# Kernel optimization log

Hardware: AMD Instinct MI355X
Metric: run time of the kernel (lower is better)

## Reference

```python
import jax, jax.numpy as jnp
import numpy as np

B, N, E, H = 32, 1024, 1024, 8
D = E // H      # head_dim = 128, att_mid_dim = [128, 64, 128]
MID = 64


def setup_inputs() -> dict:
    key = jax.random.key(0)
    ks = jax.random.split(key, 12)

    def lin(k, out_d, in_d):
        return (jax.random.normal(k, (out_d, in_d), jnp.float32) * 0.02,
                jnp.zeros((out_d,), jnp.float32))

    Wq, bq = lin(ks[0], E, E)
    Wk, bk = lin(ks[1], E, E)
    Wv, bv = lin(ks[2], E, E)
    Wb, bb = lin(ks[3], MID, D)    # attention_basic: Linear(mid[0]=D -> mid[1]=64) + ReLU
    Wl, bl = lin(ks[4], 1, MID)    # attention_last: Linear(64 -> 1)
    Wl2, bl2 = lin(ks[5], D, MID)  # attention_last2: Linear(64 -> D)
    query = jax.random.normal(ks[6], (B, E), jnp.float32)
    k_in = jax.random.normal(ks[7], (B, N, E), jnp.float32)
    value1 = jax.random.normal(ks[8], (B, E), jnp.float32)
    value2 = jax.random.normal(ks[9], (B, N, E), jnp.float32)
    mask = jax.random.randint(ks[10], (B, N), 0, 2, jnp.int32)
    mask = mask.at[:, 0].set(1)  # guarantee at least one valid position per row
    return {"query": query, "key": k_in, "mask": mask, "value1": value1,
            "value2": value2, "Wq": Wq, "bq": bq, "Wk": Wk, "bk": bk,
            "Wv": Wv, "bv": bv, "Wb": Wb, "bb": bb, "Wl": Wl, "bl": bl,
            "Wl2": Wl2, "bl2": bl2}


def reference(query, key, mask, value1, value2, Wq, bq, Wk, bk, Wv, bv,
              Wb, bb, Wl, bl, Wl2, bl2):
    # --- QKV projections (single-query attention) ---
    Q = (query @ Wq.T + bq).reshape(B, 1, H, D).transpose(0, 2, 1, 3)    # [B,H,1,D]
    K = (key @ Wk.T + bk).reshape(B, N, H, D).transpose(0, 2, 1, 3)      # [B,H,N,D]
    V = (key @ Wv.T + bv).reshape(B, N, H, D).transpose(0, 2, 1, 3)      # [B,H,N,D]
    v1 = value1.reshape(B, H, D)                                          # [B,H,D]
    v2 = (value2 @ Wv.T + bv).reshape(B, N, H, D).transpose(0, 2, 1, 3)   # [B,H,N,D]

    scores = jnp.einsum('bhqd,bhkd->bhqk', Q, K) / jnp.sqrt(jnp.float32(D))  # [B,H,1,N]
    attended = jnp.einsum('bhqk,bhkd->bhqd', scores, V)                      # [B,H,1,D]
    attn_map = jnp.broadcast_to(attended, (B, H, N, D))                      # expand(-1,-1,N,-1)

    # --- SCAtt attn_net ---
    h = jax.nn.relu(jnp.einsum('bhnd,md->bhnm', attn_map, Wb) + bb)          # [B,H,N,64]
    mf = mask.astype(h.dtype)                                                # [B,N]
    mext = mf[:, None, :, None]                                              # [B,1,N,1]
    att_map_pool = jnp.sum(h * mext, axis=2) / jnp.sum(mext, axis=2)         # [B,H,64]
    alpha_spatial = (jnp.einsum('bhnm,om->bhno', h, Wl) + bl)[..., 0]        # [B,H,N]
    alpha_channel = jax.nn.sigmoid(att_map_pool @ Wl2.T + bl2)               # [B,H,D]
    alpha_spatial = jnp.where(mf[:, None, :] == 0, jnp.float32(-1e9), alpha_spatial)
    alpha_spatial = jax.nn.softmax(alpha_spatial, axis=-1)                   # [B,H,N]
    v2_att = jnp.einsum('bhn,bhnd->bhd', alpha_spatial, v2)                  # [B,H,D]
    attn = v1 * v2_att * alpha_channel                                       # [B,H,D]
    return attn.reshape(B, H * D)
```

## Files before the change

kernel.cpp:

```cpp
#include <hip/hip_runtime.h>

#define B_  32
#define N_  1024
#define E_  1024
#define H_  8
#define D_  128
#define MID_ 64
#define NT_  16
#define TR_  64
#define NS2_ 16


__global__ __launch_bounds__(256) void k_qkproj(
        const float* __restrict__ query, const float* __restrict__ Wq,
        const float* __restrict__ bq, const float* __restrict__ Wk,
        const float* __restrict__ bk, float* __restrict__ qk,
        float* __restrict__ qb)
{
    const int bh = blockIdx.x;
    const int b = bh >> 3, h = bh & 7;
    const int t = threadIdx.x;

    __shared__ float Qp[2][D_];
    __shared__ float Qs[D_];
    __shared__ float red[2];

    {
        const int d = t & 127, half = t >> 7;
        const int row = h * D_ + d;
        const float4* wr = (const float4*)(Wq + (size_t)row * E_) + half * 128;
        const float4* qr = (const float4*)(query + (size_t)b * E_) + half * 128;
        float acc = 0.f;
        for (int i = 0; i < 128; ++i) {
            float4 w = wr[i], q = qr[i];
            acc += w.x * q.x + w.y * q.y + w.z * q.z + w.w * q.w;
        }
        Qp[half][d] = acc;
    }
    __syncthreads();
    if (t < D_) {
        const int row = h * D_ + t;
        float q = Qp[0][t] + Qp[1][t] + bq[row];
        Qs[t] = q;
        float qp = q * bk[row];
        #pragma unroll
        for (int off = 32; off; off >>= 1) qp += __shfl_down(qp, off);
        if ((t & 63) == 0) red[t >> 6] = qp;
    }
    __syncthreads();
    if (t == 0) qb[bh] = red[0] + red[1];

    const int e0 = t * 4;
    float4 a = make_float4(0.f, 0.f, 0.f, 0.f);
    const float* wkb = Wk + (size_t)(h * D_) * E_ + e0;
    for (int d = 0; d < D_; ++d) {
        float Qd = Qs[d];
        float4 w = *(const float4*)(wkb + (size_t)d * E_);
        a.x += Qd * w.x; a.y += Qd * w.y; a.z += Qd * w.z; a.w += Qd * w.w;
    }
    *(float4*)(qk + (size_t)bh * E_ + e0) = a;
}

__global__ __launch_bounds__(256) void k_scorepool(
        const float* __restrict__ key, const float* __restrict__ qk,
        const float* __restrict__ qb, float* __restrict__ PP,
        float* __restrict__ ssum)
{
    const int tile = blockIdx.x, b = blockIdx.y;
    const int t = threadIdx.x;
    const int c = t & 31, g = t >> 5;

    __shared__ __align__(16) float qks[H_ * E_];
    __shared__ __align__(16) float ssc[TR_][H_];

    {
        const float4* src = (const float4*)(qk + (size_t)b * H_ * E_);
        float4* dst = (float4*)qks;
        #pragma unroll
        for (int k = 0; k < 8; ++k) dst[t + k * 256] = src[t + k * 256];
    }
    __syncthreads();

    const float scale = 0.08838834764831845f;
    const float* keyb = key + ((size_t)b * N_ + (size_t)tile * TR_) * E_;
    const float4* qks4 = (const float4*)qks;
    const float qbv = qb[b * 8 + (c & 7)];

    float tsum = 0.f;
    #pragma unroll
    for (int p = 0; p < 2; ++p) {
        float acc[H_][4];
        #pragma unroll
        for (int h = 0; h < H_; ++h)
            #pragma unroll
            for (int j = 0; j < 4; ++j) acc[h][j] = 0.f;

        const float4* kr[4];
        #pragma unroll
        for (int j = 0; j < 4; ++j)
            kr[j] = (const float4*)(keyb + (size_t)(p * 32 + g * 4 + j) * E_);

        #pragma unroll 4
        for (int i = 0; i < 8; ++i) {
            float4 kf[4];
            #pragma unroll
            for (int j = 0; j < 4; ++j) kf[j] = kr[j][i * 32 + c];
            #pragma unroll
            for (int h = 0; h < H_; ++h) {
                float4 qf = qks4[h * 256 + i * 32 + c];
                #pragma unroll
                for (int j = 0; j < 4; ++j) {
                    acc[h][j] += qf.x * kf[j].x + qf.y * kf[j].y
                               + qf.z * kf[j].z + qf.w * kf[j].w;
                }
            }
        }
        #pragma unroll
        for (int off = 16; off; off >>= 1) {
            #pragma unroll
            for (int h = 0; h < H_; ++h)
                #pragma unroll
                for (int j = 0; j < 4; ++j)
                    acc[h][j] += __shfl_xor(acc[h][j], off);
        }
        const int r0 = p * 32 + g * 4;
        #pragma unroll
        for (int h = 0; h < H_; ++h) {
            if (c == h) {
                #pragma unroll
                for (int j = 0; j < 4; ++j) {
                    float s = (acc[h][j] + qbv) * scale;
                    ssc[r0 + j][h] = s;
                    tsum += s;
                }
            }
        }
    }
    if (c < H_) atomicAdd(&ssum[b * 8 + c], tsum);
    __syncthreads();

    {
        const int e0 = t * 4;
        float pacc[H_][4] = {};
        const float* kb = keyb + e0;
        #pragma unroll 4
        for (int n = 0; n < TR_; ++n) {
            float4 kv = *(const float4*)(kb + (size_t)n * E_);
            float4 s0 = *(const float4*)&ssc[n][0];
            float4 s1 = *(const float4*)&ssc[n][4];
            pacc[0][0] += s0.x * kv.x; pacc[0][1] += s0.x * kv.y;
            pacc[0][2] += s0.x * kv.z; pacc[0][3] += s0.x * kv.w;
            pacc[1][0] += s0.y * kv.x; pacc[1][1] += s0.y * kv.y;
            pacc[1][2] += s0.y * kv.z; pacc[1][3] += s0.y * kv.w;
            pacc[2][0] += s0.z * kv.x; pacc[2][1] += s0.z * kv.y;
            pacc[2][2] += s0.z * kv.z; pacc[2][3] += s0.z * kv.w;
            pacc[3][0] += s0.w * kv.x; pacc[3][1] += s0.w * kv.y;
            pacc[3][2] += s0.w * kv.z; pacc[3][3] += s0.w * kv.w;
            pacc[4][0] += s1.x * kv.x; pacc[4][1] += s1.x * kv.y;
            pacc[4][2] += s1.x * kv.z; pacc[4][3] += s1.x * kv.w;
            pacc[5][0] += s1.y * kv.x; pacc[5][1] += s1.y * kv.y;
            pacc[5][2] += s1.y * kv.z; pacc[5][3] += s1.y * kv.w;
            pacc[6][0] += s1.z * kv.x; pacc[6][1] += s1.z * kv.y;
            pacc[6][2] += s1.z * kv.z; pacc[6][3] += s1.z * kv.w;
            pacc[7][0] += s1.w * kv.x; pacc[7][1] += s1.w * kv.y;
            pacc[7][2] += s1.w * kv.z; pacc[7][3] += s1.w * kv.w;
        }
        #pragma unroll
        for (int h = 0; h < H_; ++h) {
            float* dst = PP + ((size_t)(b * H_) + h) * E_ + e0;
            atomicAdd(dst + 0, pacc[h][0]); atomicAdd(dst + 1, pacc[h][1]);
            atomicAdd(dst + 2, pacc[h][2]); atomicAdd(dst + 3, pacc[h][3]);
        }
    }
}

__global__ __launch_bounds__(256) void k_pool_v2(
        const float* __restrict__ value2, const int* __restrict__ mask,
        float* __restrict__ P2)
{
    const int ns = blockIdx.x, b = blockIdx.y;
    const int t = threadIdx.x, e0 = t * 4;
    const int n0 = ns * (N_ / NS2_);

    __shared__ int rows[N_ / NS2_];
    __shared__ int nrows;
    if (t == 0) nrows = 0;
    __syncthreads();
    if (t < N_ / NS2_) {
        if (mask[b * N_ + n0 + t]) {
            int idx = atomicAdd(&nrows, 1);
            rows[idx] = t;
        }
    }
    __syncthreads();
    const int nr = nrows;

    float a0 = 0.f, a1 = 0.f, a2 = 0.f, a3 = 0.f;
    const float* vb = value2 + ((size_t)(b * N_ + n0)) * E_ + e0;
    for (int i = 0; i < nr; ++i) {
        float4 v = *(const float4*)(vb + (size_t)rows[i] * E_);
        a0 += v.x; a1 += v.y; a2 += v.z; a3 += v.w;
    }
    float* dst = P2 + (size_t)b * E_ + e0;
    atomicAdd(dst + 0, a0); atomicAdd(dst + 1, a1);
    atomicAdd(dst + 2, a2); atomicAdd(dst + 3, a3);
}

__global__ __launch_bounds__(256) void k_final(
        const float* __restrict__ PP, const float* __restrict__ P2,
        const float* __restrict__ ssumg, const int* __restrict__ mask,
        const float* __restrict__ Wv, const float* __restrict__ bv,
        const float* __restrict__ Wb, const float* __restrict__ bb,
        const float* __restrict__ Wl2, const float* __restrict__ bl2,
        const float* __restrict__ value1, float* __restrict__ out)
{
    const int bh = blockIdx.x, b = bh >> 3, h = bh & 7;
    const int t = threadIdx.x;
    const int d = t & 127, half = t >> 7;

    __shared__ __align__(16) float pooled[E_];
    __shared__ __align__(16) float pool2[E_];
    __shared__ float attA[2][D_];
    __shared__ float attV[2][D_];
    __shared__ float att[D_];
    __shared__ float hv[MID_];
    __shared__ float red2[4];
    __shared__ float cnt_s;

    {
        const float4* pp = (const float4*)(PP + ((size_t)(b * H_) + h) * E_);
        const float4* p2 = (const float4*)(P2 + (size_t)b * E_);
        ((float4*)pooled)[t] = pp[t];
        ((float4*)pool2)[t]  = p2[t];

        int ci = 0;
        #pragma unroll
        for (int i = 0; i < 4; ++i) ci += mask[b * N_ + t + i * 256];
        float cf = (float)ci;
        #pragma unroll
        for (int off = 32; off; off >>= 1) cf += __shfl_down(cf, off);
        if ((t & 63) == 0) red2[t >> 6] = cf;
    }
    __syncthreads();
    if (t == 0) cnt_s = red2[0] + red2[1] + red2[2] + red2[3];

    const float ss = ssumg[bh];
    const float4* wv = (const float4*)(Wv + ((size_t)(h * D_ + d)) * E_) + half * 128;
    float accA = 0.f, accV = 0.f;
    #pragma unroll 4
    for (int i = 0; i < 128; ++i) {
        float4 w = wv[i];
        float4 pa = ((const float4*)pooled)[half * 128 + i];
        float4 pb = ((const float4*)pool2)[half * 128 + i];
        accA += pa.x * w.x + pa.y * w.y + pa.z * w.z + pa.w * w.w;
        accV += pb.x * w.x + pb.y * w.y + pb.z * w.z + pb.w * w.w;
    }
    attA[half][d] = accA;
    attV[half][d] = accV;
    __syncthreads();
    const float cnt = cnt_s;
    if (t < D_) att[t] = attA[0][t] + attA[1][t] + ss * bv[h * D_ + t];
    __syncthreads();
    if (t < MID_) {
        float a = bb[t];
        #pragma unroll 4
        for (int d2 = 0; d2 < D_; ++d2) a += att[d2] * Wb[t * D_ + d2];
        hv[t] = fmaxf(a, 0.f);
    }
    __syncthreads();
    if (t < D_) {
        float z = bl2[t];
        #pragma unroll
        for (int m = 0; m < MID_; ++m) z += hv[m] * Wl2[t * MID_ + m];
        float alphac = 1.f / (1.f + expf(-z));
        const float bvd = bv[h * D_ + t];
        float v2a = (attV[0][t] + attV[1][t]) / cnt + bvd;
        out[(size_t)b * E_ + h * D_ + t] =
            value1[(size_t)b * E_ + h * D_ + t] * v2a * alphac;
    }
}

extern "C" void kernel_launch(void* const* d_in, const int* in_sizes, int n_in,
                              void* d_out, int out_size, void* d_ws, size_t ws_size,
                              hipStream_t stream)
{
    const float* query  = (const float*)d_in[0];
    const float* key    = (const float*)d_in[1];
    const int*   mask   = (const int*)d_in[2];
    const float* value1 = (const float*)d_in[3];
    const float* value2 = (const float*)d_in[4];
    const float* Wq  = (const float*)d_in[5];
    const float* bq  = (const float*)d_in[6];
    const float* Wk  = (const float*)d_in[7];
    const float* bk  = (const float*)d_in[8];
    const float* Wv  = (const float*)d_in[9];
    const float* bv  = (const float*)d_in[10];
    const float* Wb  = (const float*)d_in[11];
    const float* bb  = (const float*)d_in[12];
    const float* Wl2 = (const float*)d_in[15];
    const float* bl2 = (const float*)d_in[16];
    float* out = (float*)d_out;

    char* ws = (char*)d_ws;
    const size_t OFF_P2 = (size_t)B_ * H_ * E_ * 4;
    const size_t OFF_SS = OFF_P2 + (size_t)B_ * E_ * 4;
    const size_t OFF_QB = OFF_SS + 1024;
    const size_t OFF_QK = OFF_QB + 1024;
    float* PP   = (float*)(ws);
    float* P2   = (float*)(ws + OFF_P2);
    float* ssum = (float*)(ws + OFF_SS);
    float* qb   = (float*)(ws + OFF_QB);
    float* qk   = (float*)(ws + OFF_QK);

    hipMemsetAsync(d_ws, 0, OFF_QB, stream);

    hipLaunchKernelGGL(k_qkproj, dim3(B_ * H_), dim3(256), 0, stream,
                       query, Wq, bq, Wk, bk, qk, qb);
    hipLaunchKernelGGL(k_scorepool, dim3(NT_, B_), dim3(256), 0, stream,
                       key, qk, qb, PP, ssum);
    hipLaunchKernelGGL(k_pool_v2, dim3(NS2_, B_), dim3(256), 0, stream,
                       value2, mask, P2);
    hipLaunchKernelGGL(k_final, dim3(B_ * H_), dim3(256), 0, stream,
                       PP, P2, ssum, mask, Wv, bv, Wb, bb, Wl2, bl2, value1, out);
}
```

Before: 437.5 us.

## Fuse v2 pooling into projection kernel, widen score tiles, coalesce final GEMV

Merges the value2 masked-pooling kernel into the Q/K projection kernel as extra blocks, so the two independent stages share one launch and can overlap. The score stage now computes 8 key rows per thread group in one pass instead of two passes of 4, which raises register pressure but reuses each shared-memory qk load across more rows. The final kernel's Wv GEMV is reorganised so 16 lanes read consecutive float4s of a row and reduce with shuffles, giving coalesced weight reads. Together these aim to cut launch overhead and memory stalls.

```diff
diff --git a/kernel.cpp b/kernel.cpp
--- a/kernel.cpp
+++ b/kernel.cpp
@@ -11,54 +11,90 @@
 #define NS2_ 16
 
 
-__global__ __launch_bounds__(256) void k_qkproj(
+__global__ __launch_bounds__(256) void k_pre(
         const float* __restrict__ query, const float* __restrict__ Wq,
         const float* __restrict__ bq, const float* __restrict__ Wk,
         const float* __restrict__ bk, float* __restrict__ qk,
-        float* __restrict__ qb)
+        float* __restrict__ qb,
+        const float* __restrict__ value2, const int* __restrict__ mask,
+        float* __restrict__ P2)
 {
-    const int bh = blockIdx.x;
-    const int b = bh >> 3, h = bh & 7;
     const int t = threadIdx.x;
 
     __shared__ float Qp[2][D_];
     __shared__ float Qs[D_];
     __shared__ float red[2];
-
-    {
-        const int d = t & 127, half = t >> 7;
-        const int row = h * D_ + d;
-        const float4* wr = (const float4*)(Wq + (size_t)row * E_) + half * 128;
-        const float4* qr = (const float4*)(query + (size_t)b * E_) + half * 128;
-        float acc = 0.f;
-        for (int i = 0; i < 128; ++i) {
-            float4 w = wr[i], q = qr[i];
-            acc += w.x * q.x + w.y * q.y + w.z * q.z + w.w * q.w;
-        }
-        Qp[half][d] = acc;
-    }
-    __syncthreads();
-    if (t < D_) {
-        const int row = h * D_ + t;
-        float q = Qp[0][t] + Qp[1][t] + bq[row];
-        Qs[t] = q;
-        float qp = q * bk[row];
-        #pragma unroll
-        for (int off = 32; off; off >>= 1) qp += __shfl_down(qp, off);
-        if ((t & 63) == 0) red[t >> 6] = qp;
-    }
-    __syncthreads();
-    if (t == 0) qb[bh] = red[0] + red[1];
-
-    const int e0 = t * 4;
-    float4 a = make_float4(0.f, 0.f, 0.f, 0.f);
-    const float* wkb = Wk + (size_t)(h * D_) * E_ + e0;
-    for (int d = 0; d < D_; ++d) {
-        float Qd = Qs[d];
-        float4 w = *(const float4*)(wkb + (size_t)d * E_);
-        a.x += Qd * w.x; a.y += Qd * w.y; a.z += Qd * w.z; a.w += Qd * w.w;
-    }
-    *(float4*)(qk + (size_t)bh * E_ + e0) = a;
+    __shared__ int rows[N_ / NS2_];
+    __shared__ int nrows;
+
+    if (blockIdx.x < 256) {
+        const int bh = blockIdx.x;
+        const int b = bh >> 3, h = bh & 7;
+
+        {
+            const int d = t & 127, half = t >> 7;
+            const int row = h * D_ + d;
+            const float4* wr = (const float4*)(Wq + (size_t)row * E_) + half * 128;
+            const float4* qr = (const float4*)(query + (size_t)b * E_) + half * 128;
+            float acc = 0.f;
+            #pragma unroll 8
+            for (int i = 0; i < 128; ++i) {
+                float4 w = wr[i], q = qr[i];
+                acc += w.x * q.x + w.y * q.y + w.z * q.z + w.w * q.w;
+            }
+            Qp[half][d] = acc;
+        }
+        __syncthreads();
+        if (t < D_) {
+            const int row = h * D_ + t;
+            float q = Qp[0][t] + Qp[1][t] + bq[row];
+            Qs[t] = q;
+            float qp = q * bk[row];
+            #pragma unroll
+            for (int off = 32; off; off >>= 1) qp += __shfl_down(qp, off);
+            if ((t & 63) == 0) red[t >> 6] = qp;
+        }
+        __syncthreads();
+        if (t == 0) qb[bh] = red[0] + red[1];
+
+        const int e0 = t * 4;
+        float4 a = make_float4(0.f, 0.f, 0.f, 0.f);
+        const float* wkb = Wk + (size_t)(h * D_) * E_ + e0;
+        #pragma unroll 8
+        for (int d = 0; d < D_; ++d) {
+            float Qd = Qs[d];
+            float4 w = *(const float4*)(wkb + (size_t)d * E_);
+            a.x += Qd * w.x; a.y += Qd * w.y; a.z += Qd * w.z; a.w += Qd * w.w;
+        }
+        *(float4*)(qk + (size_t)bh * E_ + e0) = a;
+    } else {
+        const int idx = blockIdx.x - 256;
+        const int b = idx & 31, ns = idx >> 5;
+        const int e0 = t * 4;
+        const int n0 = ns * (N_ / NS2_);
+
+        if (t == 0) nrows = 0;
+        __syncthreads();
+        if (t < N_ / NS2_) {
+            if (mask[b * N_ + n0 + t]) {
+                int i2 = atomicAdd(&nrows, 1);
+                rows[i2] = t;
+            }
+        }
+        __syncthreads();
+        const int nr = nrows;
+
+        float a0 = 0.f, a1 = 0.f, a2 = 0.f, a3 = 0.f;
+        const float* vb = value2 + ((size_t)(b * N_ + n0)) * E_ + e0;
+        #pragma unroll 4
+        for (int i = 0; i < nr; ++i) {
+            float4 v = *(const float4*)(vb + (size_t)rows[i] * E_);
+            a0 += v.x; a1 += v.y; a2 += v.z; a3 += v.w;
+        }
+        float* dst = P2 + (size_t)b * E_ + e0;
+        atomicAdd(dst + 0, a0); atomicAdd(dst + 1, a1);
+        atomicAdd(dst + 2, a2); atomicAdd(dst + 3, a3);
+    }
 }
 
 __global__ __launch_bounds__(256) void k_scorepool(
@@ -86,53 +122,49 @@
     const float4* qks4 = (const float4*)qks;
     const float qbv = qb[b * 8 + (c & 7)];
 
+    float acc[H_][8];
+    #pragma unroll
+    for (int h = 0; h < H_; ++h)
+        #pragma unroll
+        for (int j = 0; j < 8; ++j) acc[h][j] = 0.f;
+
+    const float4* kr[8];
+    #pragma unroll
+    for (int j = 0; j < 8; ++j)
+        kr[j] = (const float4*)(keyb + (size_t)(g * 8 + j) * E_);
+
+    #pragma unroll 2
+    for (int i = 0; i < 8; ++i) {
+        float4 kf[8];
+        #pragma unroll
+        for (int j = 0; j < 8; ++j) kf[j] = kr[j][i * 32 + c];
+        #pragma unroll
+        for (int h = 0; h < H_; ++h) {
+            float4 qf = qks4[h * 256 + i * 32 + c];
+            #pragma unroll
+            for (int j = 0; j < 8; ++j) {
+                acc[h][j] += qf.x * kf[j].x + qf.y * kf[j].y
+                           + qf.z * kf[j].z + qf.w * kf[j].w;
+            }
+        }
+    }
+    #pragma unroll
+    for (int off = 16; off; off >>= 1) {
+        #pragma unroll
+        for (int h = 0; h < H_; ++h)
+            #pragma unroll
+            for (int j = 0; j < 8; ++j)
+                acc[h][j] += __shfl_xor(acc[h][j], off);
+    }
     float tsum = 0.f;
     #pragma unroll
-    for (int p = 0; p < 2; ++p) {
-        float acc[H_][4];
-        #pragma unroll
-        for (int h = 0; h < H_; ++h)
+    for (int h = 0; h < H_; ++h) {
+        if (c == h) {
             #pragma unroll
-            for (int j = 0; j < 4; ++j) acc[h][j] = 0.f;
-
-        const float4* kr[4];
-        #pragma unroll
-        for (int j = 0; j < 4; ++j)
-            kr[j] = (const float4*)(keyb + (size_t)(p * 32 + g * 4 + j) * E_);
-
-        #pragma unroll 4
-        for (int i = 0; i < 8; ++i) {
-            float4 kf[4];
-            #pragma unroll
-            for (int j = 0; j < 4; ++j) kf[j] = kr[j][i * 32 + c];
-            #pragma unroll
-            for (int h = 0; h < H_; ++h) {
-                float4 qf = qks4[h * 256 + i * 32 + c];
-                #pragma unroll
-                for (int j = 0; j < 4; ++j) {
-                    acc[h][j] += qf.x * kf[j].x + qf.y * kf[j].y
-                               + qf.z * kf[j].z + qf.w * kf[j].w;
-                }
-            }
-        }
-        #pragma unroll
-        for (int off = 16; off; off >>= 1) {
-            #pragma unroll
-            for (int h = 0; h < H_; ++h)
-                #pragma unroll
-                for (int j = 0; j < 4; ++j)
-                    acc[h][j] += __shfl_xor(acc[h][j], off);
-        }
-        const int r0 = p * 32 + g * 4;
-        #pragma unroll
-        for (int h = 0; h < H_; ++h) {
-            if (c == h) {
-                #pragma unroll
-                for (int j = 0; j < 4; ++j) {
-                    float s = (acc[h][j] + qbv) * scale;
-                    ssc[r0 + j][h] = s;
-                    tsum += s;
-                }
+            for (int j = 0; j < 8; ++j) {
+                float s = (acc[h][j] + qbv) * scale;
+                ssc[g * 8 + j][h] = s;
+                tsum += s;
             }
         }
     }
@@ -174,38 +206,6 @@
     }
 }
 
-__global__ __launch_bounds__(256) void k_pool_v2(
-        const float* __restrict__ value2, const int* __restrict__ mask,
-        float* __restrict__ P2)
-{
-    const int ns = blockIdx.x, b = blockIdx.y;
-    const int t = threadIdx.x, e0 = t * 4;
-    const int n0 = ns * (N_ / NS2_);
-
-    __shared__ int rows[N_ / NS2_];
-    __shared__ int nrows;
-    if (t == 0) nrows = 0;
-    __syncthreads();
-    if (t < N_ / NS2_) {
-        if (mask[b * N_ + n0 + t]) {
-            int idx = atomicAdd(&nrows, 1);
-            rows[idx] = t;
-        }
-    }
-    __syncthreads();
-    const int nr = nrows;
-
-    float a0 = 0.f, a1 = 0.f, a2 = 0.f, a3 = 0.f;
-    const float* vb = value2 + ((size_t)(b * N_ + n0)) * E_ + e0;
-    for (int i = 0; i < nr; ++i) {
-        float4 v = *(const float4*)(vb + (size_t)rows[i] * E_);
-        a0 += v.x; a1 += v.y; a2 += v.z; a3 += v.w;
-    }
-    float* dst = P2 + (size_t)b * E_ + e0;
-    atomicAdd(dst + 0, a0); atomicAdd(dst + 1, a1);
-    atomicAdd(dst + 2, a2); atomicAdd(dst + 3, a3);
-}
-
 __global__ __launch_bounds__(256) void k_final(
         const float* __restrict__ PP, const float* __restrict__ P2,
         const float* __restrict__ ssumg, const int* __restrict__ mask,
@@ -216,12 +216,13 @@
 {
     const int bh = blockIdx.x, b = bh >> 3, h = bh & 7;
     const int t = threadIdx.x;
-    const int d = t & 127, half = t >> 7;
+    const int l = t & 63, w = t >> 6;
+    const int rg = l >> 4, cl = l & 15;
 
     __shared__ __align__(16) float pooled[E_];
     __shared__ __align__(16) float pool2[E_];
-    __shared__ float attA[2][D_];
-    __shared__ float attV[2][D_];
+    __shared__ float attA_s[D_];
+    __shared__ float attV_s[D_];
     __shared__ float att[D_];
     __shared__ float hv[MID_];
     __shared__ float red2[4];
@@ -239,27 +240,37 @@
         float cf = (float)ci;
         #pragma unroll
         for (int off = 32; off; off >>= 1) cf += __shfl_down(cf, off);
-        if ((t & 63) == 0) red2[t >> 6] = cf;
+        if (l == 0) red2[w] = cf;
     }
     __syncthreads();
     if (t == 0) cnt_s = red2[0] + red2[1] + red2[2] + red2[3];
 
+    const float4* pooled4 = (const float4*)pooled;
+    const float4* pool24  = (const float4*)pool2;
+    #pragma unroll 2
+    for (int pass = 0; pass < 8; ++pass) {
+        const int d = pass * 16 + w * 4 + rg;
+        const float4* wvr = (const float4*)(Wv + (size_t)(h * D_ + d) * E_);
+        float pA = 0.f, pV = 0.f;
+        #pragma unroll 4
+        for (int i = 0; i < 16; ++i) {
+            float4 wv4 = wvr[cl + i * 16];
+            float4 pa = pooled4[cl + i * 16];
+            float4 pb = pool24[cl + i * 16];
+            pA += wv4.x * pa.x + wv4.y * pa.y + wv4.z * pa.z + wv4.w * pa.w;
+            pV += wv4.x * pb.x + wv4.y * pb.y + wv4.z * pb.z + wv4.w * pb.w;
+        }
+        #pragma unroll
+        for (int off = 8; off; off >>= 1) {
+            pA += __shfl_xor(pA, off);
+            pV += __shfl_xor(pV, off);
+        }
+        if (cl == 0) { attA_s[d] = pA; attV_s[d] = pV; }
+    }
+    __syncthreads();
+    const float cnt = cnt_s;
     const float ss = ssumg[bh];
-    const float4* wv = (const float4*)(Wv + ((size_t)(h * D_ + d)) * E_) + half * 128;
-    float accA = 0.f, accV = 0.f;
-    #pragma unroll 4
-    for (int i = 0; i < 128; ++i) {
-        float4 w = wv[i];
-        float4 pa = ((const float4*)pooled)[half * 128 + i];
-        float4 pb = ((const float4*)pool2)[half * 128 + i];
-        accA += pa.x * w.x + pa.y * w.y + pa.z * w.z + pa.w * w.w;
-        accV += pb.x * w.x + pb.y * w.y + pb.z * w.z + pb.w * w.w;
-    }
-    attA[half][d] = accA;
-    attV[half][d] = accV;
-    __syncthreads();
-    const float cnt = cnt_s;
-    if (t < D_) att[t] = attA[0][t] + attA[1][t] + ss * bv[h * D_ + t];
+    if (t < D_) att[t] = attA_s[t] + ss * bv[h * D_ + t];
     __syncthreads();
     if (t < MID_) {
         float a = bb[t];
@@ -274,7 +285,7 @@
         for (int m = 0; m < MID_; ++m) z += hv[m] * Wl2[t * MID_ + m];
         float alphac = 1.f / (1.f + expf(-z));
         const float bvd = bv[h * D_ + t];
-        float v2a = (attV[0][t] + attV[1][t]) / cnt + bvd;
+        float v2a = attV_s[t] / cnt + bvd;
         out[(size_t)b * E_ + h * D_ + t] =
             value1[(size_t)b * E_ + h * D_ + t] * v2a * alphac;
     }
@@ -314,12 +325,10 @@
 
     hipMemsetAsync(d_ws, 0, OFF_QB, stream);
 
-    hipLaunchKernelGGL(k_qkproj, dim3(B_ * H_), dim3(256), 0, stream,
-                       query, Wq, bq, Wk, bk, qk, qb);
+    hipLaunchKernelGGL(k_pre, dim3(256 + NS2_ * B_), dim3(256), 0, stream,
+                       query, Wq, bq, Wk, bk, qk, qb, value2, mask, P2);
     hipLaunchKernelGGL(k_scorepool, dim3(NT_, B_), dim3(256), 0, stream,
                        key, qk, qb, PP, ssum);
-    hipLaunchKernelGGL(k_pool_v2, dim3(NS2_, B_), dim3(256), 0, stream,
-                       value2, mask, P2);
     hipLaunchKernelGGL(k_final, dim3(B_ * H_), dim3(256), 0, stream,
                        PP, P2, ssum, mask, Wv, bv, Wb, bb, Wl2, bl2, value1, out);
 }
```

Measured after the change: 427.0 us. -2.4%, faster.
